# Optimization experiments

Hardware: AMD Instinct MI355X
Metric: run time of the kernel (lower is better)

Reference implementation:

```python
import jax, jax.numpy as jnp
import numpy as np

N_NODES = 50000
N_EDGES = 800000
IN_DIM = 256
NHID = 64
OUT_DIM = 64
DEPTH = 4
P = 2.0


def _gcn_conv(x, W, b, src, dst, n):
    # PyG GCNConv: xW, add self-loops, sym-normalize, aggregate src->dst, + bias
    xw = x @ W
    loop = jnp.arange(n)
    s = jnp.concatenate([src, loop])
    d = jnp.concatenate([dst, loop])
    deg = jax.ops.segment_sum(jnp.ones_like(d, dtype=xw.dtype), d, num_segments=n)
    dis = jnp.where(deg > 0, jax.lax.rsqrt(jnp.maximum(deg, 1.0)), 0.0)
    w = dis[s] * dis[d]  # [E+n]
    out = jax.ops.segment_sum(w[:, None] * xw[s], d, num_segments=n)
    return out + b


def _g2_gate(x, W, b, src, dst, n):
    xg = jax.nn.relu(_gcn_conv(x, W, b, src, dst, n))
    diff = jnp.abs(xg[src] - xg[dst]) ** P  # [E, nhid]
    sums = jax.ops.segment_sum(diff, src, num_segments=n)
    cnt = jax.ops.segment_sum(jnp.ones((src.shape[0],), dtype=x.dtype), src, num_segments=n)
    return jnp.tanh(sums / jnp.maximum(cnt, 1.0)[:, None])


def setup_inputs() -> dict:
    key = jax.random.key(0)
    ks = jax.random.split(key, 10)
    x = jax.random.normal(ks[0], (N_NODES, IN_DIM), dtype=jnp.float32)
    edge_index = jax.random.randint(ks[1], (2, N_EDGES), 0, N_NODES, dtype=jnp.int64 if jax.config.jax_enable_x64 else jnp.int32)
    s = 0.05
    return {
        "x": x,
        "edge_index": edge_index,
        "enc_w": jax.random.normal(ks[2], (IN_DIM, NHID), dtype=jnp.float32) * s,
        "enc_b": jnp.zeros((NHID,), dtype=jnp.float32),
        "conv_w": jax.random.normal(ks[3], (NHID, NHID), dtype=jnp.float32) * s,
        "conv_b": jnp.zeros((NHID,), dtype=jnp.float32),
        "gg_w": jax.random.normal(ks[4], (NHID, NHID), dtype=jnp.float32) * s,
        "gg_b": jnp.zeros((NHID,), dtype=jnp.float32),
        "dec_w": jax.random.normal(ks[5], (NHID, OUT_DIM), dtype=jnp.float32) * s,
        "dec_b": jnp.zeros((OUT_DIM,), dtype=jnp.float32),
    }


def reference(x, edge_index, enc_w, enc_b, conv_w, conv_b, gg_w, gg_b, dec_w, dec_b):
    n = x.shape[0]
    src, dst = edge_index[0], edge_index[1]
    # eval mode: dropouts are identity
    X = jax.nn.relu(x @ enc_w + enc_b)
    for _ in range(DEPTH):
        X_ = jax.nn.relu(_gcn_conv(X, conv_w, conv_b, src, dst, n))
        tau = _g2_gate(X, gg_w, gg_b, src, dst, n)
        X = (1.0 - tau) * X + tau * X_
    X = jax.nn.relu(X @ dec_w + dec_b)
    return X
```

## Files before the change

kernel.cpp:

```cpp
#include <hip/hip_runtime.h>
#include <math.h>

#define NN 50000
#define NE 800000
#define IND 256
#define NH 64
#define DEPTH 4
#define PART_DIV 6250
#define SB 49
#define CEB 782


__device__ __forceinline__ unsigned short f2bf(float f) {
    unsigned int x = __float_as_uint(f);
    unsigned int r = (x + 0x7fffu + ((x >> 16) & 1u)) >> 16;
    return (unsigned short)r;
}
__device__ __forceinline__ unsigned int pack2bf(float lo, float hi) {
    return (unsigned int)f2bf(lo) | ((unsigned int)f2bf(hi) << 16);
}
__device__ __forceinline__ ushort4 f4_to_us4(float4 f) {
    ushort4 u;
    u.x = f2bf(f.x); u.y = f2bf(f.y); u.z = f2bf(f.z); u.w = f2bf(f.w);
    return u;
}
__device__ __forceinline__ void acc8(float* a, uint4 r) {
    a[0] += __uint_as_float(r.x << 16); a[1] += __uint_as_float(r.x & 0xffff0000u);
    a[2] += __uint_as_float(r.y << 16); a[3] += __uint_as_float(r.y & 0xffff0000u);
    a[4] += __uint_as_float(r.z << 16); a[5] += __uint_as_float(r.z & 0xffff0000u);
    a[6] += __uint_as_float(r.w << 16); a[7] += __uint_as_float(r.w & 0xffff0000u);
}
__device__ __forceinline__ void unpack8(float* a, uint4 r) {
    a[0] = __uint_as_float(r.x << 16); a[1] = __uint_as_float(r.x & 0xffff0000u);
    a[2] = __uint_as_float(r.y << 16); a[3] = __uint_as_float(r.y & 0xffff0000u);
    a[4] = __uint_as_float(r.z << 16); a[5] = __uint_as_float(r.z & 0xffff0000u);
    a[6] = __uint_as_float(r.w << 16); a[7] = __uint_as_float(r.w & 0xffff0000u);
}
__device__ __forceinline__ void accd8(float* a, const float* xg, uint4 r) {
    float e;
    e = xg[0] - __uint_as_float(r.x << 16);         a[0] += e * e;
    e = xg[1] - __uint_as_float(r.x & 0xffff0000u); a[1] += e * e;
    e = xg[2] - __uint_as_float(r.y << 16);         a[2] += e * e;
    e = xg[3] - __uint_as_float(r.y & 0xffff0000u); a[3] += e * e;
    e = xg[4] - __uint_as_float(r.z << 16);         a[4] += e * e;
    e = xg[5] - __uint_as_float(r.z & 0xffff0000u); a[5] += e * e;
    e = xg[6] - __uint_as_float(r.w << 16);         a[6] += e * e;
    e = xg[7] - __uint_as_float(r.w & 0xffff0000u); a[7] += e * e;
}
__device__ __forceinline__ float tanh_pos(float x) {
    float t = __expf(-2.f * x);
    return (1.f - t) / (1.f + t);
}

__global__ __launch_bounds__(256) void count_enc(
    const int* __restrict__ src, const int* __restrict__ dst,
    int* __restrict__ degin, int* __restrict__ degout,
    int* __restrict__ rank_in, int* __restrict__ rank_out,
    const float* __restrict__ x, const float* __restrict__ enc_w,
    const float* __restrict__ enc_b, float* __restrict__ X)
{
    __shared__ float Ws[64 * 64];
    __shared__ float Xs[64][68];
    int bid = blockIdx.x;
    if ((bid & 1) == 0) {
        int c = bid >> 1;
        for (int e = c * 256 + threadIdx.x; e < NE; e += CEB * 256) {
            int s = src[e], d = dst[e];
            rank_in[e]  = atomicAdd(&degin[d], 1);
            rank_out[e] = atomicAdd(&degout[s], 1);
        }
        return;
    }
    int tid = threadIdx.x;
    int row0 = (bid >> 1) * 64;
    int r16 = tid >> 4;
    int cg = tid & 15;
    float4 acc[4];
#pragma unroll
    for (int t = 0; t < 4; ++t) acc[t] = make_float4(0.f, 0.f, 0.f, 0.f);

    for (int kc = 0; kc < IND; kc += 64) {
        const float4* W4 = (const float4*)(enc_w + (size_t)kc * 64);
        float4* Ws4 = (float4*)Ws;
#pragma unroll
        for (int t = 0; t < 4; ++t) Ws4[tid + t * 256] = W4[tid + t * 256];
#pragma unroll
        for (int t = 0; t < 4; ++t) {
            int r = r16 + t * 16;
            int grow = row0 + r;
            float4 xv = make_float4(0.f, 0.f, 0.f, 0.f);
            if (grow < NN) xv = *(const float4*)(x + (size_t)grow * IND + kc + cg * 4);
            Xs[r][cg * 4 + 0] = xv.x; Xs[r][cg * 4 + 1] = xv.y;
            Xs[r][cg * 4 + 2] = xv.z; Xs[r][cg * 4 + 3] = xv.w;
        }
        __syncthreads();
#pragma unroll
        for (int k = 0; k < 64; ++k) {
            float4 w4 = ((const float4*)Ws)[k * 16 + cg];
#pragma unroll
            for (int t = 0; t < 4; ++t) {
                float xv = Xs[r16 + t * 16][k];
                acc[t].x += xv * w4.x; acc[t].y += xv * w4.y;
                acc[t].z += xv * w4.z; acc[t].w += xv * w4.w;
            }
        }
        __syncthreads();
    }
    float4 b4 = ((const float4*)enc_b)[cg];
#pragma unroll
    for (int t = 0; t < 4; ++t) {
        int row = row0 + r16 + t * 16;
        if (row < NN) {
            float4 o;
            o.x = fmaxf(acc[t].x + b4.x, 0.f); o.y = fmaxf(acc[t].y + b4.y, 0.f);
            o.z = fmaxf(acc[t].z + b4.z, 0.f); o.w = fmaxf(acc[t].w + b4.w, 0.f);
            ((float4*)(X + (size_t)row * 64))[cg] = o;
        }
    }
}

__global__ __launch_bounds__(512) void scan_p1(const int* __restrict__ in0,
                                               const int* __restrict__ in1,
                                               int* __restrict__ tmp,
                                               int* __restrict__ bsum) {
    int a = blockIdx.x / SB;
    int b = blockIdx.x % SB;
    const int* in = a ? in1 : in0;
    int t = threadIdx.x;
    int base = b * 1024 + t * 2;
    int v0 = (base < NN) ? in[base] : 0;
    int v1 = (base + 1 < NN) ? in[base + 1] : 0;
    int v = v0 + v1;
    int x = v;
#pragma unroll
    for (int off = 1; off < 64; off <<= 1) {
        int u = __shfl_up(x, off);
        if ((t & 63) >= off) x += u;
    }
    __shared__ int ws[8];
    int wid = t >> 6, lane = t & 63;
    if (lane == 63) ws[wid] = x;
    __syncthreads();
    if (t == 0) {
        int run = 0;
#pragma unroll
        for (int w = 0; w < 8; ++w) { int s = ws[w]; ws[w] = run; run += s; }
    }
    __syncthreads();
    x += ws[wid];
    int excl = x - v;
    if (base < NN) tmp[a * NN + base] = excl;
    if (base + 1 < NN) tmp[a * NN + base + 1] = excl + v0;
    if (t == 511) bsum[a * SB + b] = x;
}

__global__ __launch_bounds__(128) void scan_p2(int* __restrict__ bsum,
                                               int* __restrict__ out0,
                                               int* __restrict__ out1) {
    int t = threadIdx.x;
    int a = t >> 6, lane = t & 63;
    int v = (lane < SB) ? bsum[a * SB + lane] : 0;
    int x = v;
#pragma unroll
    for (int off = 1; off < 64; off <<= 1) {
        int u = __shfl_up(x, off);
        if (lane >= off) x += u;
    }
    if (lane < SB) bsum[a * SB + lane] = x - v;
    if (lane == SB - 1) {
        if (a == 0) out0[NN] = x; else out1[NN] = x;
    }
}

__global__ __launch_bounds__(512) void scan_p3(const int* __restrict__ tmp,
                                               const int* __restrict__ bsum,
                                               int* __restrict__ out0,
                                               int* __restrict__ out1) {
    int a = blockIdx.x / SB;
    int b = blockIdx.x % SB;
    int* out = a ? out1 : out0;
    int add = bsum[a * SB + b];
    int t = threadIdx.x;
    int base = b * 1024 + t * 2;
    if (base < NN) out[base] = tmp[a * NN + base] + add;
    if (base + 1 < NN) out[base + 1] = tmp[a * NN + base + 1] + add;
}

__global__ __launch_bounds__(256) void init_pack(
    const int* __restrict__ degin, const int* __restrict__ degout,
    float* __restrict__ dis, float* __restrict__ cntf,
    const float* __restrict__ X, unsigned short* __restrict__ Xbf)
{
    int t = blockIdx.x * 256 + threadIdx.x;
    int node = t >> 3, l8 = t & 7;
    if (node >= NN) return;
    float di = rsqrtf((float)(degin[node] + 1));
    if (l8 == 0) {
        dis[node] = di;
        int od = degout[node];
        cntf[node] = (float)(od > 0 ? od : 1);
    }
    const float4* xp = (const float4*)(X + (size_t)node * 64 + l8 * 8);
    float4 v0 = xp[0], v1 = xp[1];
    uint4 pk;
    pk.x = pack2bf(v0.x * di, v0.y * di);
    pk.y = pack2bf(v0.z * di, v0.w * di);
    pk.z = pack2bf(v1.x * di, v1.y * di);
    pk.w = pack2bf(v1.z * di, v1.w * di);
    ((uint4*)Xbf)[(size_t)node * 8 + l8] = pk;
}

__global__ void bucket_hist(const int* __restrict__ degin, const int* __restrict__ degout,
                            int* __restrict__ ghin, int* __restrict__ ghout) {
    __shared__ int lin[128], lout[128];
    int t = threadIdx.x;
    if (t < 128) { lin[t] = 0; lout[t] = 0; }
    __syncthreads();
    int i = blockIdx.x * 256 + t;
    if (i < NN) {
        atomicAdd(&lin[min(degin[i], 127)], 1);
        atomicAdd(&lout[min(degout[i], 127)], 1);
    }
    __syncthreads();
    if (t < 128) {
        if (lin[t])  atomicAdd(&ghin[t],  lin[t]);
        if (lout[t]) atomicAdd(&ghout[t], lout[t]);
    }
}

__global__ void bucket_scan(const int* __restrict__ ghin, const int* __restrict__ ghout,
                            int* __restrict__ curin, int* __restrict__ curout) {
    __shared__ int a[128], b[128];
    int t = threadIdx.x;
    if (t < 128) a[t] = ghin[t]; else b[t - 128] = ghout[t - 128];
    __syncthreads();
    if (t == 0) { int run = 0; for (int k = 0; k < 128; ++k) { int v = a[k]; a[k] = run; run += v; } }
    if (t == 1) { int run = 0; for (int k = 0; k < 128; ++k) { int v = b[k]; b[k] = run; run += v; } }
    __syncthreads();
    if (t < 128) curin[t] = a[t]; else curout[t - 128] = b[t - 128];
}

__global__ void bucket_scatter(const int* __restrict__ degin, const int* __restrict__ degout,
                               int* __restrict__ curin, int* __restrict__ curout,
                               int* __restrict__ order_in, int* __restrict__ order_out) {
    __shared__ int lin[128], lout[128], basein[128], baseout[128];
    int t = threadIdx.x;
    if (t < 128) { lin[t] = 0; lout[t] = 0; }
    __syncthreads();
    int i = blockIdx.x * 256 + t;
    int bi = 0, bo = 0, ri = 0, ro = 0;
    if (i < NN) {
        bi = min(degin[i], 127);  ri = atomicAdd(&lin[bi], 1);
        bo = min(degout[i], 127); ro = atomicAdd(&lout[bo], 1);
    }
    __syncthreads();
    if (t < 128) {
        basein[t]  = lin[t]  ? atomicAdd(&curin[t],  lin[t])  : 0;
        baseout[t] = lout[t] ? atomicAdd(&curout[t], lout[t]) : 0;
    }
    __syncthreads();
    if (i < NN) {
        order_in[basein[bi] + ri] = i;
        order_out[baseout[bo] + ro] = i;
    }
}

__global__ void fill_csr_part(const int* __restrict__ src, const int* __restrict__ dst,
                              const int* __restrict__ off_dst, const int* __restrict__ off_src,
                              const int* __restrict__ rank_in, const int* __restrict__ rank_out,
                              int* __restrict__ srcs_by_dst, int* __restrict__ dsts_by_src,
                              int nGroups) {
    int q = blockIdx.x & 7;
    int g = blockIdx.x >> 3;
    for (int e = g * 256 + threadIdx.x; e < NE; e += nGroups * 256) {
        int s = src[e], d = dst[e];
        if (d / PART_DIV == q) srcs_by_dst[off_dst[d] + rank_in[e]] = s;
        if (s / PART_DIV == q) dsts_by_src[off_src[s] + rank_out[e]] = d;
    }
}

template<int K>
__global__ __launch_bounds__(256) void gemm64b(const float* __restrict__ X,
                                               const float* __restrict__ W,
                                               const float* __restrict__ bias,
                                               float* __restrict__ out, int n) {
    __shared__ float Ws[64 * 64];
    __shared__ float Xs[64][68];
    int tid = threadIdx.x;
    int row0 = blockIdx.x * 64;
    int r16 = tid >> 4;
    int cg = tid & 15;
    float4 acc[4];
#pragma unroll
    for (int t = 0; t < 4; ++t) acc[t] = make_float4(0.f, 0.f, 0.f, 0.f);

    for (int kc = 0; kc < K; kc += 64) {
        const float4* W4 = (const float4*)(W + (size_t)kc * 64);
        float4* Ws4 = (float4*)Ws;
#pragma unroll
        for (int t = 0; t < 4; ++t) Ws4[tid + t * 256] = W4[tid + t * 256];
#pragma unroll
        for (int t = 0; t < 4; ++t) {
            int r = r16 + t * 16;
            int grow = row0 + r;
            float4 xv = make_float4(0.f, 0.f, 0.f, 0.f);
            if (grow < n) xv = *(const float4*)(X + (size_t)grow * K + kc + cg * 4);
            Xs[r][cg * 4 + 0] = xv.x; Xs[r][cg * 4 + 1] = xv.y;
            Xs[r][cg * 4 + 2] = xv.z; Xs[r][cg * 4 + 3] = xv.w;
        }
        __syncthreads();
#pragma unroll
        for (int k = 0; k < 64; ++k) {
            float4 w4 = ((const float4*)Ws)[k * 16 + cg];
#pragma unroll
            for (int t = 0; t < 4; ++t) {
                float xv = Xs[r16 + t * 16][k];
                acc[t].x += xv * w4.x; acc[t].y += xv * w4.y;
                acc[t].z += xv * w4.z; acc[t].w += xv * w4.w;
            }
        }
        __syncthreads();
    }

    float4 b4 = ((const float4*)bias)[cg];
#pragma unroll
    for (int t = 0; t < 4; ++t) {
        int row = row0 + r16 + t * 16;
        if (row < n) {
            float4 o;
            o.x = fmaxf(acc[t].x + b4.x, 0.f); o.y = fmaxf(acc[t].y + b4.y, 0.f);
            o.z = fmaxf(acc[t].z + b4.z, 0.f); o.w = fmaxf(acc[t].w + b4.w, 0.f);
            ((float4*)(out + (size_t)row * 64))[cg] = o;
        }
    }
}

__global__ __launch_bounds__(256) void dualgemm32(
    const float* __restrict__ Z,
    const float* __restrict__ Wb, const float* __restrict__ bb,
    const float* __restrict__ Wc, const float* __restrict__ bc,
    unsigned short* __restrict__ Bbf, unsigned short* __restrict__ Cbf, int n)
{
    __shared__ float W2[64 * 128];
    __shared__ float Xs[32][68];
    int tid = threadIdx.x;
    int row0 = blockIdx.x * 32;
    {
        const float4* wb4 = (const float4*)Wb;
        const float4* wc4 = (const float4*)Wc;
#pragma unroll
        for (int t = 0; t < 4; ++t) {
            int idx = tid + t * 256;
            int k = idx >> 4, c = (idx & 15) * 4;
            *(float4*)&W2[k * 128 + c]      = wb4[idx];
            *(float4*)&W2[k * 128 + 64 + c] = wc4[idx];
        }
#pragma unroll
        for (int t = 0; t < 2; ++t) {
            int idx = tid + t * 256;
            int r = idx >> 4, c4 = idx & 15;
            int gr = row0 + r;
            float4 xv = make_float4(0.f, 0.f, 0.f, 0.f);
            if (gr < n) xv = *(const float4*)(Z + (size_t)gr * 64 + c4 * 4);
            Xs[r][c4 * 4 + 0] = xv.x; Xs[r][c4 * 4 + 1] = xv.y;
            Xs[r][c4 * 4 + 2] = xv.z; Xs[r][c4 * 4 + 3] = xv.w;
        }
    }
    __syncthreads();

    int r8 = tid >> 5;
    int cg = tid & 31;
    float4 acc[4];
#pragma unroll
    for (int t = 0; t < 4; ++t) acc[t] = make_float4(0.f, 0.f, 0.f, 0.f);
#pragma unroll
    for (int k = 0; k < 64; ++k) {
        float4 w4 = *(const float4*)&W2[k * 128 + cg * 4];
#pragma unroll
        for (int t = 0; t < 4; ++t) {
            float xv = Xs[r8 + t * 8][k];
            acc[t].x += xv * w4.x; acc[t].y += xv * w4.y;
            acc[t].z += xv * w4.z; acc[t].w += xv * w4.w;
        }
    }

    float4 bv = (cg < 16) ? ((const float4*)bb)[cg] : ((const float4*)bc)[cg - 16];
#pragma unroll
    for (int t = 0; t < 4; ++t) {
        int row = row0 + r8 + t * 8;
        if (row < n) {
            float4 o;
            o.x = fmaxf(acc[t].x + bv.x, 0.f); o.y = fmaxf(acc[t].y + bv.y, 0.f);
            o.z = fmaxf(acc[t].z + bv.z, 0.f); o.w = fmaxf(acc[t].w + bv.w, 0.f);
            if (cg < 16) ((ushort4*)(Bbf + (size_t)row * 64))[cg]      = f4_to_us4(o);
            else         ((ushort4*)(Cbf + (size_t)row * 64))[cg - 16] = f4_to_us4(o);
        }
    }
}

__global__ __launch_bounds__(256) void zgather(
    const unsigned short* __restrict__ Xbf,
    const int* __restrict__ off, const int* __restrict__ nbr,
    const float* __restrict__ dis, const int* __restrict__ order,
    float* __restrict__ Z)
{
    int t = blockIdx.x * 256 + threadIdx.x;
    int idx = t >> 3, l8 = t & 7;
    if (idx >= NN) return;
    int node = order[idx];
    const uint4* Xb = (const uint4*)Xbf;
    float a[8];
    unpack8(a, Xb[(size_t)node * 8 + l8]);
    int lo = off[node], hi = off[node + 1];
    int j = lo;
    for (; j + 7 < hi; j += 8) {
        int s0 = nbr[j],     s1 = nbr[j + 1], s2 = nbr[j + 2], s3 = nbr[j + 3];
        int s4 = nbr[j + 4], s5 = nbr[j + 5], s6 = nbr[j + 6], s7 = nbr[j + 7];
        uint4 r0 = Xb[(size_t)s0 * 8 + l8];
        uint4 r1 = Xb[(size_t)s1 * 8 + l8];
        uint4 r2 = Xb[(size_t)s2 * 8 + l8];
        uint4 r3 = Xb[(size_t)s3 * 8 + l8];
        uint4 r4 = Xb[(size_t)s4 * 8 + l8];
        uint4 r5 = Xb[(size_t)s5 * 8 + l8];
        uint4 r6 = Xb[(size_t)s6 * 8 + l8];
        uint4 r7 = Xb[(size_t)s7 * 8 + l8];
        acc8(a, r0); acc8(a, r1); acc8(a, r2); acc8(a, r3);
        acc8(a, r4); acc8(a, r5); acc8(a, r6); acc8(a, r7);
    }
    for (; j + 3 < hi; j += 4) {
        int s0 = nbr[j], s1 = nbr[j + 1], s2 = nbr[j + 2], s3 = nbr[j + 3];
        uint4 r0 = Xb[(size_t)s0 * 8 + l8];
        uint4 r1 = Xb[(size_t)s1 * 8 + l8];
        uint4 r2 = Xb[(size_t)s2 * 8 + l8];
        uint4 r3 = Xb[(size_t)s3 * 8 + l8];
        acc8(a, r0); acc8(a, r1); acc8(a, r2); acc8(a, r3);
    }
    for (; j < hi; ++j) {
        acc8(a, Xb[(size_t)nbr[j] * 8 + l8]);
    }
    float di = dis[node];
    float* zp = Z + (size_t)node * 64 + l8 * 8;
    *(float4*)(zp)     = make_float4(di * a[0], di * a[1], di * a[2], di * a[3]);
    *(float4*)(zp + 4) = make_float4(di * a[4], di * a[5], di * a[6], di * a[7]);
}

__global__ __launch_bounds__(256) void gate_update8(
    const unsigned short* __restrict__ Cbf, const unsigned short* __restrict__ Xnbf,
    float* __restrict__ X, unsigned short* __restrict__ Xbf,
    const int* __restrict__ off, const int* __restrict__ nbr,
    const float* __restrict__ cntf, const float* __restrict__ dis,
    const int* __restrict__ order)
{
    int t = blockIdx.x * 256 + threadIdx.x;
    int idx = t >> 3, l8 = t & 7;
    if (idx >= NN) return;
    int node = order[idx];
    const uint4* Cb = (const uint4*)Cbf;
    float xg[8];
    unpack8(xg, Cb[(size_t)node * 8 + l8]);
    float a[8] = {0.f, 0.f, 0.f, 0.f, 0.f, 0.f, 0.f, 0.f};
    int lo = off[node], hi = off[node + 1];
    int j = lo;
    for (; j + 7 < hi; j += 8) {
        int d0 = nbr[j],     d1 = nbr[j + 1], d2 = nbr[j + 2], d3 = nbr[j + 3];
        int d4 = nbr[j + 4], d5 = nbr[j + 5], d6 = nbr[j + 6], d7 = nbr[j + 7];
        uint4 r0 = Cb[(size_t)d0 * 8 + l8];
        uint4 r1 = Cb[(size_t)d1 * 8 + l8];
        uint4 r2 = Cb[(size_t)d2 * 8 + l8];
        uint4 r3 = Cb[(size_t)d3 * 8 + l8];
        uint4 r4 = Cb[(size_t)d4 * 8 + l8];
        uint4 r5 = Cb[(size_t)d5 * 8 + l8];
        uint4 r6 = Cb[(size_t)d6 * 8 + l8];
        uint4 r7 = Cb[(size_t)d7 * 8 + l8];
        accd8(a, xg, r0); accd8(a, xg, r1); accd8(a, xg, r2); accd8(a, xg, r3);
        accd8(a, xg, r4); accd8(a, xg, r5); accd8(a, xg, r6); accd8(a, xg, r7);
    }
    for (; j + 3 < hi; j += 4) {
        int d0 = nbr[j], d1 = nbr[j + 1], d2 = nbr[j + 2], d3 = nbr[j + 3];
        uint4 r0 = Cb[(size_t)d0 * 8 + l8];
        uint4 r1 = Cb[(size_t)d1 * 8 + l8];
        uint4 r2 = Cb[(size_t)d2 * 8 + l8];
        uint4 r3 = Cb[(size_t)d3 * 8 + l8];
        accd8(a, xg, r0); accd8(a, xg, r1); accd8(a, xg, r2); accd8(a, xg, r3);
    }
    for (; j < hi; ++j) {
        accd8(a, xg, Cb[(size_t)nbr[j] * 8 + l8]);
    }
    float inv = 1.f / cntf[node];
    float di = dis[node];
    float xn[8];
    unpack8(xn, ((const uint4*)Xnbf)[(size_t)node * 8 + l8]);
    const float* xop = X + (size_t)node * 64 + l8 * 8;
    float o[8];
#pragma unroll
    for (int k = 0; k < 8; ++k) {
        float tau = tanh_pos(a[k] * inv);
        float xo = xop[k];
        o[k] = xo + tau * (xn[k] - xo);
    }
    float* xp = X + (size_t)node * 64 + l8 * 8;
    *(float4*)(xp)     = make_float4(o[0], o[1], o[2], o[3]);
    *(float4*)(xp + 4) = make_float4(o[4], o[5], o[6], o[7]);
    uint4 pk;
    pk.x = pack2bf(o[0] * di, o[1] * di);
    pk.y = pack2bf(o[2] * di, o[3] * di);
    pk.z = pack2bf(o[4] * di, o[5] * di);
    pk.w = pack2bf(o[6] * di, o[7] * di);
    ((uint4*)Xbf)[(size_t)node * 8 + l8] = pk;
}


extern "C" void kernel_launch(void* const* d_in, const int* in_sizes, int n_in,
                              void* d_out, int out_size, void* d_ws, size_t ws_size,
                              hipStream_t stream) {
    const float* x      = (const float*)d_in[0];
    const int*   ei     = (const int*)d_in[1];
    const float* enc_w  = (const float*)d_in[2];
    const float* enc_b  = (const float*)d_in[3];
    const float* conv_w = (const float*)d_in[4];
    const float* conv_b = (const float*)d_in[5];
    const float* gg_w   = (const float*)d_in[6];
    const float* gg_b   = (const float*)d_in[7];
    const float* dec_w  = (const float*)d_in[8];
    const float* dec_b  = (const float*)d_in[9];
    float* out = (float*)d_out;

    const int* src = ei;
    const int* dst = ei + NE;

    char* p = (char*)d_ws;
    auto alloc = [&](size_t bytes) -> void* {
        void* r = (void*)p;
        p += (bytes + 255) & ~(size_t)255;
        return r;
    };
    float* X   = (float*)alloc((size_t)NN * 64 * 4);
    float* Zb  = (float*)alloc((size_t)NN * 64 * 4);
    unsigned short* Bbf = (unsigned short*)alloc((size_t)NN * 64 * 2);
    unsigned short* Xbf = (unsigned short*)alloc((size_t)NN * 64 * 2);
    unsigned short* Cbf = (unsigned short*)alloc((size_t)NN * 64 * 2);
    float* dis  = (float*)alloc((size_t)NN * 4);
    float* cntf = (float*)alloc((size_t)NN * 4);
    int* degin   = (int*)alloc((size_t)NN * 4);
    int* degout  = (int*)alloc((size_t)NN * 4);
    int* off_dst = (int*)alloc((size_t)(NN + 1) * 4);
    int* off_src = (int*)alloc((size_t)(NN + 1) * 4);
    int* rank_in  = (int*)alloc((size_t)NE * 4);
    int* rank_out = (int*)alloc((size_t)NE * 4);
    int* sbd     = (int*)alloc((size_t)NE * 4);
    int* dbs     = (int*)alloc((size_t)NE * 4);
    int* stmp    = (int*)alloc((size_t)2 * NN * 4);
    int* bsum    = (int*)alloc((size_t)2 * SB * 4);
    int* order_in  = (int*)alloc((size_t)NN * 4);
    int* order_out = (int*)alloc((size_t)NN * 4);
    int* gbins   = (int*)alloc((size_t)512 * 4);
    int* ghin = gbins, *ghout = gbins + 128, *curin = gbins + 256, *curout = gbins + 384;

    hipMemsetAsync(degin, 0, (size_t)NN * 4, stream);
    hipMemsetAsync(degout, 0, (size_t)NN * 4, stream);
    hipMemsetAsync(gbins, 0, (size_t)512 * 4, stream);

    const int NB = (NN + 255) / 256;
    const int OB = ((NN * 8) + 255) / 256;
    const int NGROUPS = 104;

    count_enc<<<2 * CEB, 256, 0, stream>>>(src, dst, degin, degout,
                                           rank_in, rank_out, x, enc_w, enc_b, X);
    scan_p1<<<2 * SB, 512, 0, stream>>>(degin, degout, stmp, bsum);
    scan_p2<<<1, 128, 0, stream>>>(bsum, off_dst, off_src);
    scan_p3<<<2 * SB, 512, 0, stream>>>(stmp, bsum, off_dst, off_src);
    init_pack<<<OB, 256, 0, stream>>>(degin, degout, dis, cntf, X, Xbf);
    bucket_hist<<<NB, 256, 0, stream>>>(degin, degout, ghin, ghout);
    bucket_scan<<<1, 256, 0, stream>>>(ghin, ghout, curin, curout);
    bucket_scatter<<<NB, 256, 0, stream>>>(degin, degout, curin, curout,
                                           order_in, order_out);
    fill_csr_part<<<8 * NGROUPS, 256, 0, stream>>>(src, dst, off_dst, off_src,
                                                   rank_in, rank_out, sbd, dbs, NGROUPS);

    const int GB   = (NN + 63) / 64;
    const int GB32 = (NN + 31) / 32;

    for (int l = 0; l < DEPTH; ++l) {
        zgather<<<OB, 256, 0, stream>>>(Xbf, off_dst, sbd, dis, order_in, Zb);
        dualgemm32<<<GB32, 256, 0, stream>>>(Zb, conv_w, conv_b, gg_w, gg_b, Bbf, Cbf, NN);
        gate_update8<<<OB, 256, 0, stream>>>(Cbf, Bbf, X, Xbf, off_src, dbs,
                                             cntf, dis, order_out);
    }

    gemm64b<NH><<<GB, 256, 0, stream>>>(X, dec_w, dec_b, out, NN);
}
```

Baseline: 625.7 us.

## Split bf16 feature tables into column halves and gather each half separately

```diff
diff --git a/kernel.cpp b/kernel.cpp
--- a/kernel.cpp
+++ b/kernel.cpp
@@ -189,7 +189,8 @@
 __global__ __launch_bounds__(256) void init_pack(
     const int* __restrict__ degin, const int* __restrict__ degout,
     float* __restrict__ dis, float* __restrict__ cntf,
-    const float* __restrict__ X, unsigned short* __restrict__ Xbf)
+    const float* __restrict__ X,
+    unsigned short* __restrict__ XbfLo, unsigned short* __restrict__ XbfHi)
 {
     int t = blockIdx.x * 256 + threadIdx.x;
     int node = t >> 3, l8 = t & 7;
@@ -207,7 +208,8 @@
     pk.y = pack2bf(v0.z * di, v0.w * di);
     pk.z = pack2bf(v1.x * di, v1.y * di);
     pk.w = pack2bf(v1.z * di, v1.w * di);
-    ((uint4*)Xbf)[(size_t)node * 8 + l8] = pk;
+    unsigned short* tbl = (l8 < 4) ? XbfLo : XbfHi;
+    ((uint4*)tbl)[(size_t)node * 4 + (l8 & 3)] = pk;
 }
 
 __global__ void bucket_hist(const int* __restrict__ degin, const int* __restrict__ degout,
@@ -339,7 +341,8 @@
     const float* __restrict__ Z,
     const float* __restrict__ Wb, const float* __restrict__ bb,
     const float* __restrict__ Wc, const float* __restrict__ bc,
-    unsigned short* __restrict__ Bbf, unsigned short* __restrict__ Cbf, int n)
+    unsigned short* __restrict__ Bbf,
+    unsigned short* __restrict__ CbfLo, unsigned short* __restrict__ CbfHi, int n)
 {
     __shared__ float W2[64 * 128];
     __shared__ float Xs[32][68];
@@ -392,105 +395,110 @@
             float4 o;
             o.x = fmaxf(acc[t].x + bv.x, 0.f); o.y = fmaxf(acc[t].y + bv.y, 0.f);
             o.z = fmaxf(acc[t].z + bv.z, 0.f); o.w = fmaxf(acc[t].w + bv.w, 0.f);
-            if (cg < 16) ((ushort4*)(Bbf + (size_t)row * 64))[cg]      = f4_to_us4(o);
-            else         ((ushort4*)(Cbf + (size_t)row * 64))[cg - 16] = f4_to_us4(o);
-        }
-    }
-}
-
-__global__ __launch_bounds__(256) void zgather(
-    const unsigned short* __restrict__ Xbf,
+            if (cg < 16) {
+                ((ushort4*)(Bbf + (size_t)row * 64))[cg] = f4_to_us4(o);
+            } else {
+                int c = (cg - 16) * 4;
+                if (c < 32) ((ushort4*)(CbfLo + (size_t)row * 32))[c >> 2] = f4_to_us4(o);
+                else        ((ushort4*)(CbfHi + (size_t)row * 32))[(c - 32) >> 2] = f4_to_us4(o);
+            }
+        }
+    }
+}
+
+__global__ __launch_bounds__(256) void zgather_h(
+    const unsigned short* __restrict__ Xh,
     const int* __restrict__ off, const int* __restrict__ nbr,
     const float* __restrict__ dis, const int* __restrict__ order,
-    float* __restrict__ Z)
+    float* __restrict__ Z, int h)
 {
     int t = blockIdx.x * 256 + threadIdx.x;
-    int idx = t >> 3, l8 = t & 7;
+    int idx = t >> 2, l4 = t & 3;
     if (idx >= NN) return;
     int node = order[idx];
-    const uint4* Xb = (const uint4*)Xbf;
+    const uint4* Xb = (const uint4*)Xh;
     float a[8];
-    unpack8(a, Xb[(size_t)node * 8 + l8]);
+    unpack8(a, Xb[(size_t)node * 4 + l4]);
     int lo = off[node], hi = off[node + 1];
     int j = lo;
     for (; j + 7 < hi; j += 8) {
         int s0 = nbr[j],     s1 = nbr[j + 1], s2 = nbr[j + 2], s3 = nbr[j + 3];
         int s4 = nbr[j + 4], s5 = nbr[j + 5], s6 = nbr[j + 6], s7 = nbr[j + 7];
-        uint4 r0 = Xb[(size_t)s0 * 8 + l8];
-        uint4 r1 = Xb[(size_t)s1 * 8 + l8];
-        uint4 r2 = Xb[(size_t)s2 * 8 + l8];
-        uint4 r3 = Xb[(size_t)s3 * 8 + l8];
-        uint4 r4 = Xb[(size_t)s4 * 8 + l8];
-        uint4 r5 = Xb[(size_t)s5 * 8 + l8];
-        uint4 r6 = Xb[(size_t)s6 * 8 + l8];
-        uint4 r7 = Xb[(size_t)s7 * 8 + l8];
+        uint4 r0 = Xb[(size_t)s0 * 4 + l4];
+        uint4 r1 = Xb[(size_t)s1 * 4 + l4];
+        uint4 r2 = Xb[(size_t)s2 * 4 + l4];
+        uint4 r3 = Xb[(size_t)s3 * 4 + l4];
+        uint4 r4 = Xb[(size_t)s4 * 4 + l4];
+        uint4 r5 = Xb[(size_t)s5 * 4 + l4];
+        uint4 r6 = Xb[(size_t)s6 * 4 + l4];
+        uint4 r7 = Xb[(size_t)s7 * 4 + l4];
         acc8(a, r0); acc8(a, r1); acc8(a, r2); acc8(a, r3);
         acc8(a, r4); acc8(a, r5); acc8(a, r6); acc8(a, r7);
     }
     for (; j + 3 < hi; j += 4) {
         int s0 = nbr[j], s1 = nbr[j + 1], s2 = nbr[j + 2], s3 = nbr[j + 3];
-        uint4 r0 = Xb[(size_t)s0 * 8 + l8];
-        uint4 r1 = Xb[(size_t)s1 * 8 + l8];
-        uint4 r2 = Xb[(size_t)s2 * 8 + l8];
-        uint4 r3 = Xb[(size_t)s3 * 8 + l8];
+        uint4 r0 = Xb[(size_t)s0 * 4 + l4];
+        uint4 r1 = Xb[(size_t)s1 * 4 + l4];
+        uint4 r2 = Xb[(size_t)s2 * 4 + l4];
+        uint4 r3 = Xb[(size_t)s3 * 4 + l4];
         acc8(a, r0); acc8(a, r1); acc8(a, r2); acc8(a, r3);
     }
     for (; j < hi; ++j) {
-        acc8(a, Xb[(size_t)nbr[j] * 8 + l8]);
+        acc8(a, Xb[(size_t)nbr[j] * 4 + l4]);
     }
     float di = dis[node];
-    float* zp = Z + (size_t)node * 64 + l8 * 8;
+    float* zp = Z + (size_t)node * 64 + h * 32 + l4 * 8;
     *(float4*)(zp)     = make_float4(di * a[0], di * a[1], di * a[2], di * a[3]);
     *(float4*)(zp + 4) = make_float4(di * a[4], di * a[5], di * a[6], di * a[7]);
 }
 
-__global__ __launch_bounds__(256) void gate_update8(
-    const unsigned short* __restrict__ Cbf, const unsigned short* __restrict__ Xnbf,
-    float* __restrict__ X, unsigned short* __restrict__ Xbf,
+__global__ __launch_bounds__(256) void gate_h(
+    const unsigned short* __restrict__ Ch, const unsigned short* __restrict__ Bbf,
+    float* __restrict__ X, unsigned short* __restrict__ XhOut,
     const int* __restrict__ off, const int* __restrict__ nbr,
     const float* __restrict__ cntf, const float* __restrict__ dis,
-    const int* __restrict__ order)
+    const int* __restrict__ order, int h)
 {
     int t = blockIdx.x * 256 + threadIdx.x;
-    int idx = t >> 3, l8 = t & 7;
+    int idx = t >> 2, l4 = t & 3;
     if (idx >= NN) return;
     int node = order[idx];
-    const uint4* Cb = (const uint4*)Cbf;
+    const uint4* Cb = (const uint4*)Ch;
     float xg[8];
-    unpack8(xg, Cb[(size_t)node * 8 + l8]);
+    unpack8(xg, Cb[(size_t)node * 4 + l4]);
     float a[8] = {0.f, 0.f, 0.f, 0.f, 0.f, 0.f, 0.f, 0.f};
     int lo = off[node], hi = off[node + 1];
     int j = lo;
     for (; j + 7 < hi; j += 8) {
         int d0 = nbr[j],     d1 = nbr[j + 1], d2 = nbr[j + 2], d3 = nbr[j + 3];
         int d4 = nbr[j + 4], d5 = nbr[j + 5], d6 = nbr[j + 6], d7 = nbr[j + 7];
-        uint4 r0 = Cb[(size_t)d0 * 8 + l8];
-        uint4 r1 = Cb[(size_t)d1 * 8 + l8];
-        uint4 r2 = Cb[(size_t)d2 * 8 + l8];
-        uint4 r3 = Cb[(size_t)d3 * 8 + l8];
-        uint4 r4 = Cb[(size_t)d4 * 8 + l8];
-        uint4 r5 = Cb[(size_t)d5 * 8 + l8];
-        uint4 r6 = Cb[(size_t)d6 * 8 + l8];
-        uint4 r7 = Cb[(size_t)d7 * 8 + l8];
+        uint4 r0 = Cb[(size_t)d0 * 4 + l4];
+        uint4 r1 = Cb[(size_t)d1 * 4 + l4];
+        uint4 r2 = Cb[(size_t)d2 * 4 + l4];
+        uint4 r3 = Cb[(size_t)d3 * 4 + l4];
+        uint4 r4 = Cb[(size_t)d4 * 4 + l4];
+        uint4 r5 = Cb[(size_t)d5 * 4 + l4];
+        uint4 r6 = Cb[(size_t)d6 * 4 + l4];
+        uint4 r7 = Cb[(size_t)d7 * 4 + l4];
         accd8(a, xg, r0); accd8(a, xg, r1); accd8(a, xg, r2); accd8(a, xg, r3);
         accd8(a, xg, r4); accd8(a, xg, r5); accd8(a, xg, r6); accd8(a, xg, r7);
     }
     for (; j + 3 < hi; j += 4) {
         int d0 = nbr[j], d1 = nbr[j + 1], d2 = nbr[j + 2], d3 = nbr[j + 3];
-        uint4 r0 = Cb[(size_t)d0 * 8 + l8];
-        uint4 r1 = Cb[(size_t)d1 * 8 + l8];
-        uint4 r2 = Cb[(size_t)d2 * 8 + l8];
-        uint4 r3 = Cb[(size_t)d3 * 8 + l8];
+        uint4 r0 = Cb[(size_t)d0 * 4 + l4];
+        uint4 r1 = Cb[(size_t)d1 * 4 + l4];
+        uint4 r2 = Cb[(size_t)d2 * 4 + l4];
+        uint4 r3 = Cb[(size_t)d3 * 4 + l4];
         accd8(a, xg, r0); accd8(a, xg, r1); accd8(a, xg, r2); accd8(a, xg, r3);
     }
     for (; j < hi; ++j) {
-        accd8(a, xg, Cb[(size_t)nbr[j] * 8 + l8]);
+        accd8(a, xg, Cb[(size_t)nbr[j] * 4 + l4]);
     }
     float inv = 1.f / cntf[node];
     float di = dis[node];
     float xn[8];
-    unpack8(xn, ((const uint4*)Xnbf)[(size_t)node * 8 + l8]);
-    const float* xop = X + (size_t)node * 64 + l8 * 8;
+    unpack8(xn, *(const uint4*)(Bbf + (size_t)node * 64 + h * 32 + l4 * 8));
+    const float* xop = X + (size_t)node * 64 + h * 32 + l4 * 8;
     float o[8];
 #pragma unroll
     for (int k = 0; k < 8; ++k) {
@@ -498,7 +506,7 @@
         float xo = xop[k];
         o[k] = xo + tau * (xn[k] - xo);
     }
-    float* xp = X + (size_t)node * 64 + l8 * 8;
+    float* xp = X + (size_t)node * 64 + h * 32 + l4 * 8;
     *(float4*)(xp)     = make_float4(o[0], o[1], o[2], o[3]);
     *(float4*)(xp + 4) = make_float4(o[4], o[5], o[6], o[7]);
     uint4 pk;
@@ -506,7 +514,7 @@
     pk.y = pack2bf(o[2] * di, o[3] * di);
     pk.z = pack2bf(o[4] * di, o[5] * di);
     pk.w = pack2bf(o[6] * di, o[7] * di);
-    ((uint4*)Xbf)[(size_t)node * 8 + l8] = pk;
+    ((uint4*)XhOut)[(size_t)node * 4 + l4] = pk;
 }
 
 
@@ -536,9 +544,11 @@
     };
     float* X   = (float*)alloc((size_t)NN * 64 * 4);
     float* Zb  = (float*)alloc((size_t)NN * 64 * 4);
-    unsigned short* Bbf = (unsigned short*)alloc((size_t)NN * 64 * 2);
-    unsigned short* Xbf = (unsigned short*)alloc((size_t)NN * 64 * 2);
-    unsigned short* Cbf = (unsigned short*)alloc((size_t)NN * 64 * 2);
+    unsigned short* Bbf   = (unsigned short*)alloc((size_t)NN * 64 * 2);
+    unsigned short* XbfLo = (unsigned short*)alloc((size_t)NN * 32 * 2);
+    unsigned short* XbfHi = (unsigned short*)alloc((size_t)NN * 32 * 2);
+    unsigned short* CbfLo = (unsigned short*)alloc((size_t)NN * 32 * 2);
+    unsigned short* CbfHi = (unsigned short*)alloc((size_t)NN * 32 * 2);
     float* dis  = (float*)alloc((size_t)NN * 4);
     float* cntf = (float*)alloc((size_t)NN * 4);
     int* degin   = (int*)alloc((size_t)NN * 4);
@@ -560,8 +570,9 @@
     hipMemsetAsync(degout, 0, (size_t)NN * 4, stream);
     hipMemsetAsync(gbins, 0, (size_t)512 * 4, stream);
 
-    const int NB = (NN + 255) / 256;
-    const int OB = ((NN * 8) + 255) / 256;
+    const int NB  = (NN + 255) / 256;
+    const int OB  = ((NN * 8) + 255) / 256;
+    const int OB4 = ((NN * 4) + 255) / 256;
     const int NGROUPS = 104;
 
     count_enc<<<2 * CEB, 256, 0, stream>>>(src, dst, degin, degout,
@@ -569,7 +580,7 @@
     scan_p1<<<2 * SB, 512, 0, stream>>>(degin, degout, stmp, bsum);
     scan_p2<<<1, 128, 0, stream>>>(bsum, off_dst, off_src);
     scan_p3<<<2 * SB, 512, 0, stream>>>(stmp, bsum, off_dst, off_src);
-    init_pack<<<OB, 256, 0, stream>>>(degin, degout, dis, cntf, X, Xbf);
+    init_pack<<<OB, 256, 0, stream>>>(degin, degout, dis, cntf, X, XbfLo, XbfHi);
     bucket_hist<<<NB, 256, 0, stream>>>(degin, degout, ghin, ghout);
     bucket_scan<<<1, 256, 0, stream>>>(ghin, ghout, curin, curout);
     bucket_scatter<<<NB, 256, 0, stream>>>(degin, degout, curin, curout,
@@ -581,10 +592,14 @@
     const int GB32 = (NN + 31) / 32;
 
     for (int l = 0; l < DEPTH; ++l) {
-        zgather<<<OB, 256, 0, stream>>>(Xbf, off_dst, sbd, dis, order_in, Zb);
-        dualgemm32<<<GB32, 256, 0, stream>>>(Zb, conv_w, conv_b, gg_w, gg_b, Bbf, Cbf, NN);
-        gate_update8<<<OB, 256, 0, stream>>>(Cbf, Bbf, X, Xbf, off_src, dbs,
-                                             cntf, dis, order_out);
+        zgather_h<<<OB4, 256, 0, stream>>>(XbfLo, off_dst, sbd, dis, order_in, Zb, 0);
+        zgather_h<<<OB4, 256, 0, stream>>>(XbfHi, off_dst, sbd, dis, order_in, Zb, 1);
+        dualgemm32<<<GB32, 256, 0, stream>>>(Zb, conv_w, conv_b, gg_w, gg_b,
+                                             Bbf, CbfLo, CbfHi, NN);
+        gate_h<<<OB4, 256, 0, stream>>>(CbfLo, Bbf, X, XbfLo, off_src, dbs,
+                                        cntf, dis, order_out, 0);
+        gate_h<<<OB4, 256, 0, stream>>>(CbfHi, Bbf, X, XbfHi, off_src, dbs,
+                                        cntf, dis, order_out, 1);
     }
 
     gemm64b<NH><<<GB, 256, 0, stream>>>(X, dec_w, dec_b, out, NN);
```

After: 1.544 ms. 2.47x slower.
